# Kernel optimization log

Hardware: AMD Instinct MI355X
Metric: run time of the kernel (lower is better)

Reference implementation:

```python
import jax, jax.numpy as jnp
import numpy as np

K = 16  # nsample for knn_point

def _bn(x, g, b):
    # inference-mode BatchNorm1d folded to per-channel affine (running stats 0/1)
    return x * g[None, :, None] + b[None, :, None]

def _knn(xyz, k):
    # xyz: [B,3,N] -> idx [B,N,k] of k nearest neighbors (squared L2)
    p = xyz.transpose(0, 2, 1)                                   # [B,N,3]
    sq = jnp.sum(p * p, axis=-1)                                 # [B,N]
    d = sq[:, :, None] + sq[:, None, :] - 2.0 * jnp.einsum('bnc,bmc->bnm', p, p)
    _, idx = jax.lax.top_k(-d, k)
    return idx

def _gather(hT, idx):
    # hT: [B,N,C], idx: [B,N,K] -> [B,N,K,C]
    return jax.vmap(lambda a, i: a[i])(hT, idx)

def setup_inputs():
    key = jax.random.key(0)
    ks = jax.random.split(key, 12)
    B, N, C = 16, 2048, 128
    def w(k, shape, fan):
        return jax.random.normal(k, shape, jnp.float32) * (1.0 / np.sqrt(fan))
    o = jnp.ones; z = jnp.zeros
    return {
        'points': jax.random.normal(ks[0], (B, 6, N), jnp.float32),
        'label': jax.random.uniform(ks[1], (B, 1, 16), jnp.float32),
        'We1': w(ks[2], (C, 6), 6), 'ge1': o(C), 'be1': z(C),
        'We2': w(ks[3], (C, C), C), 'ge2': o(C), 'be2': z(C),
        'W1': w(ks[4], (3, C, C), C), 'g1': o((3, C)), 'b1': z((3, C)),
        'W2': w(ks[5], (3, C, C), C), 'g2': o((3, C)), 'b2': z((3, C)),
        'Wf': w(ks[6], (1024, 3 * C), 3 * C), 'gf': o(1024), 'bf': z(1024),
        'Wl': w(ks[7], (64, 16), 16), 'gl': o(64), 'bl': z(64),
        'Wc1': w(ks[8], (512, 3136), 3136), 'bc1': z(512), 'gc1': o(512), 'bb1': z(512),
        'Wc2': w(ks[9], (256, 512), 512), 'bc2': z(256), 'gc2': o(256), 'bb2': z(256),
        'Wc3': w(ks[10], (50, 256), 256), 'bc3': z(50),
    }

def reference(points, label, We1, ge1, be1, We2, ge2, be2, W1, g1, b1, W2, g2, b2,
              Wf, gf, bf, Wl, gl, bl, Wc1, bc1, gc1, bb1, Wc2, bc2, gc2, bb2, Wc3, bc3):
    B, _, N = points.shape
    x = points[:, :6, :]
    xyz = x[:, :3, :]
    idx = _knn(xyz, K)                                            # [B,N,16]
    # input embedding: two conv1x1 + BN + ReLU
    h = jax.nn.relu(_bn(jnp.einsum('oc,bcn->bon', We1, x), ge1, be1))
    h = jax.nn.relu(_bn(jnp.einsum('oc,bcn->bon', We2, h), ge2, be2))
    xs = []
    for i in range(3):  # PVDSA_Res blocks (simplified: conv-BN-ReLU, kNN max-agg, conv-BN + residual)
        t = jax.nn.relu(_bn(jnp.einsum('oc,bcn->bon', W1[i], h), g1[i], b1[i]))
        nbr = _gather(t.transpose(0, 2, 1), idx)                  # [B,N,K,C]
        m = nbr.max(axis=2).transpose(0, 2, 1)                    # [B,C,N]
        h = jax.nn.relu(_bn(jnp.einsum('oc,bcn->bon', W2[i], m), g2[i], b2[i]) + h)
        xs.append(h)
    xcat = jnp.concatenate(xs, axis=1)                            # [B,384,N]
    xf = jax.nn.leaky_relu(_bn(jnp.einsum('oc,bcn->bon', Wf, xcat), gf, bf), 0.2)  # [B,1024,N]
    x_max = xf.max(axis=-1)                                       # [B,1024]
    x_avg = xf.mean(axis=-1)                                      # [B,1024]
    cls = jnp.broadcast_to(label.transpose(0, 2, 1), (B, 16, N))
    lab = jax.nn.leaky_relu(_bn(jnp.einsum('oc,bcn->bon', Wl, cls), gl, bl), 0.2)  # [B,64,N]
    glob = jnp.concatenate([
        jnp.broadcast_to(x_max[:, :, None], (B, 1024, N)),
        jnp.broadcast_to(x_avg[:, :, None], (B, 1024, N)),
        lab], axis=1)
    xa = jnp.concatenate([xf, glob], axis=1)                      # [B,3136,N]
    c = jax.nn.relu(_bn(jnp.einsum('oc,bcn->bon', Wc1, xa) + bc1[None, :, None], gc1, bb1))
    c = jax.nn.relu(_bn(jnp.einsum('oc,bcn->bon', Wc2, c) + bc2[None, :, None], gc2, bb2))
    out = jnp.einsum('oc,bcn->bon', Wc3, c) + bc3[None, :, None]  # [B,50,N]
    return out
```

## Files before the change

kernel.cpp:

```cpp
#include <hip/hip_runtime.h>
#include <cstdint>
#include <cstddef>

#define DEVINL __device__ __forceinline__

typedef float    f32x4 __attribute__((ext_vector_type(4)));
typedef _Float16 f16x8 __attribute__((ext_vector_type(8)));
typedef _Float16 f16x4 __attribute__((ext_vector_type(4)));

constexpr int BB = 16, NN = 2048, MM = 32768;

constexpr size_t OFF_WE1 = 0;
constexpr size_t OFF_WE2 = OFF_WE1 + 128 * 64 * 2;
constexpr size_t OFF_W1  = OFF_WE2 + 128 * 128 * 2;
constexpr size_t OFF_W2  = OFF_W1  + 3 * 128 * 128 * 2;
constexpr size_t OFF_WF  = OFF_W2  + 3 * 128 * 128 * 2;
constexpr size_t OFF_WC1 = OFF_WF  + 1024 * 384 * 2;
constexpr size_t OFF_WC2 = OFF_WC1 + 512 * 1024 * 2;
constexpr size_t OFF_WC3 = OFF_WC2 + 256 * 512 * 2;
constexpr size_t OFF_BC2 = OFF_WC3 + 128 * 256 * 2;
constexpr size_t OFF_BC3 = OFF_BC2 + 256 * 4;
constexpr size_t OFF_CVEC= OFF_BC3 + 128 * 4;
constexpr size_t OFF_PMAX= OFF_CVEC+ 16 * 512 * 4;
constexpr size_t OFF_PSUM= OFF_PMAX+ 16 * 16 * 1024 * 4;
constexpr size_t OFF_IDX = OFF_PSUM+ 16 * 16 * 1024 * 4;
constexpr size_t OFF_R1  = 8ull << 20;
constexpr size_t OFF_X0  = OFF_R1;
constexpr size_t OFF_HT  = OFF_R1 + (4ull  << 20);
constexpr size_t OFF_TT  = OFF_R1 + (12ull << 20);
constexpr size_t OFF_MT  = OFF_R1 + (20ull << 20);
constexpr size_t OFF_C1  = OFF_R1;
constexpr size_t OFF_XCAT= OFF_R1 + (32ull << 20);
constexpr size_t OFF_C2  = OFF_XCAT;
constexpr size_t OFF_XF  = OFF_XCAT + (24ull << 20);

__global__ __launch_bounds__(256) void fold_all_kernel(
    const float* We1, const float* ge1, const float* We2, const float* ge2,
    const float* W1,  const float* g1,  const float* W2,  const float* g2,
    const float* Wf,  const float* gf,  const float* Wc1, const float* gc1,
    const float* Wc2, const float* gc2, const float* Wc3,
    const float* gc2b, const float* bc2, const float* bb2, const float* bc3,
    const float* pts, char* ws)
{
    const int bid = blockIdx.x;
    const int tid = threadIdx.x;

    if (bid == 4704) {
        ((float*)(ws + OFF_BC2))[tid] = gc2b[tid] * bc2[tid] + bb2[tid];
        return;
    }
    if (bid == 4705) {
        if (tid < 128) ((float*)(ws + OFF_BC3))[tid] = (tid < 50) ? bc3[tid] : 0.f;
        return;
    }
    if (bid >= 4706) {
        int m = (bid - 4706) * 256 + tid;
        int b = m >> 11, n = m & 2047;
        const float* ps = pts + (size_t)b * 6 * 2048 + n;
        _Float16 tmp[64];
#pragma unroll
        for (int c = 0; c < 64; ++c) tmp[c] = (_Float16)0.f;
#pragma unroll
        for (int c = 0; c < 6; ++c) tmp[c] = (_Float16)ps[(size_t)c << 11];
        _Float16* dst = (_Float16*)(ws + OFF_X0) + (size_t)m * 64;
#pragma unroll
        for (int v = 0; v < 8; ++v) *(f16x8*)(dst + v * 8) = *(const f16x8*)(tmp + v * 8);
        return;
    }

    int id, base;
    if      (bid < 32)   { id = 0;  base = 0;    }
    else if (bid < 96)   { id = 1;  base = 32;   }
    else if (bid < 160)  { id = 2;  base = 96;   }
    else if (bid < 224)  { id = 3;  base = 160;  }
    else if (bid < 288)  { id = 4;  base = 224;  }
    else if (bid < 352)  { id = 5;  base = 288;  }
    else if (bid < 416)  { id = 6;  base = 352;  }
    else if (bid < 480)  { id = 7;  base = 416;  }
    else if (bid < 2016) { id = 8;  base = 480;  }
    else if (bid < 4064) { id = 9;  base = 2016; }
    else if (bid < 4576) { id = 10; base = 4064; }
    else                 { id = 11; base = 4576; }

    const float* src = nullptr; const float* g = nullptr; _Float16* dst = nullptr;
    int O = 0, K = 0, lds = 0, Kp = 0;
    switch (id) {
        case 0:  src = We1; g = ge1; O = 128; K = 6;    lds = 6;    Kp = 64;   dst = (_Float16*)(ws + OFF_WE1); break;
        case 1:  src = We2; g = ge2; O = 128; K = 128;  lds = 128;  Kp = 128;  dst = (_Float16*)(ws + OFF_WE2); break;
        case 2: case 3: case 4: {
            int i = id - 2;
            src = W1 + (size_t)i * 16384; g = g1 + i * 128; O = 128; K = 128; lds = 128; Kp = 128;
            dst = (_Float16*)(ws + OFF_W1) + (size_t)i * 16384; break; }
        case 5: case 6: case 7: {
            int i = id - 5;
            src = W2 + (size_t)i * 16384; g = g2 + i * 128; O = 128; K = 128; lds = 128; Kp = 128;
            dst = (_Float16*)(ws + OFF_W2) + (size_t)i * 16384; break; }
        case 8:  src = Wf;  g = gf;  O = 1024; K = 384;  lds = 384;  Kp = 384;  dst = (_Float16*)(ws + OFF_WF);  break;
        case 9:  src = Wc1; g = gc1; O = 512;  K = 1024; lds = 3136; Kp = 1024; dst = (_Float16*)(ws + OFF_WC1); break;
        case 10: src = Wc2; g = gc2; O = 256;  K = 512;  lds = 512;  Kp = 512;  dst = (_Float16*)(ws + OFF_WC2); break;
        default: src = Wc3; g = nullptr; O = 50; K = 256; lds = 256; Kp = 256;  dst = (_Float16*)(ws + OFF_WC3); break;
    }
    int e = (bid - base) * 256 + tid;
    int o = e / Kp, k = e - o * Kp;
    float v = 0.f;
    if (o < O && k < K) {
        v = src[(size_t)o * lds + k];
        if (g) v *= g[o];
    }
    dst[e] = (_Float16)v;
}

DEVINL float knn_dist(const float4 pq, const float4 pm) {
    float t = pq.x * pm.x;
    t = fmaf(pq.y, pm.y, t);
    t = fmaf(pq.z, pm.z, t);
    return fmaf(-2.f, t, pm.w);
}

#define KNN_DINS(X) do { \
    const float x_ = (X); \
    d15 = __builtin_amdgcn_fmed3f(x_, d14, d15); \
    d14 = __builtin_amdgcn_fmed3f(x_, d13, d14); \
    d13 = __builtin_amdgcn_fmed3f(x_, d12, d13); \
    d12 = __builtin_amdgcn_fmed3f(x_, d11, d12); \
    d11 = __builtin_amdgcn_fmed3f(x_, d10, d11); \
    d10 = __builtin_amdgcn_fmed3f(x_, d9,  d10); \
    d9  = __builtin_amdgcn_fmed3f(x_, d8,  d9);  \
    d8  = __builtin_amdgcn_fmed3f(x_, d7,  d8);  \
    d7  = __builtin_amdgcn_fmed3f(x_, d6,  d7);  \
    d6  = __builtin_amdgcn_fmed3f(x_, d5,  d6);  \
    d5  = __builtin_amdgcn_fmed3f(x_, d4,  d5);  \
    d4  = __builtin_amdgcn_fmed3f(x_, d3,  d4);  \
    d3  = __builtin_amdgcn_fmed3f(x_, d2,  d3);  \
    d2  = __builtin_amdgcn_fmed3f(x_, d1,  d2);  \
    d1  = __builtin_amdgcn_fmed3f(x_, d0,  d1);  \
    d0  = __builtin_amdgcn_fmed3f(x_, -3.4e38f, d0); \
} while (0)

#define KNN_CE(A, B) { const float lo_ = fminf(A, B), hi_ = fmaxf(A, B); A = lo_; B = hi_; }

#define KNN_MERGE(OFF) do { \
    const float n0  = __shfl_xor(d0,  OFF), n1  = __shfl_xor(d1,  OFF), \
                n2  = __shfl_xor(d2,  OFF), n3  = __shfl_xor(d3,  OFF), \
                n4  = __shfl_xor(d4,  OFF), n5  = __shfl_xor(d5,  OFF), \
                n6  = __shfl_xor(d6,  OFF), n7  = __shfl_xor(d7,  OFF), \
                n8  = __shfl_xor(d8,  OFF), n9  = __shfl_xor(d9,  OFF), \
                n10 = __shfl_xor(d10, OFF), n11 = __shfl_xor(d11, OFF), \
                n12 = __shfl_xor(d12, OFF), n13 = __shfl_xor(d13, OFF), \
                n14 = __shfl_xor(d14, OFF), n15 = __shfl_xor(d15, OFF); \
    d0  = fminf(d0,  n15); d1  = fminf(d1,  n14); d2  = fminf(d2,  n13); d3  = fminf(d3,  n12); \
    d4  = fminf(d4,  n11); d5  = fminf(d5,  n10); d6  = fminf(d6,  n9);  d7  = fminf(d7,  n8);  \
    d8  = fminf(d8,  n7);  d9  = fminf(d9,  n6);  d10 = fminf(d10, n5);  d11 = fminf(d11, n4);  \
    d12 = fminf(d12, n3);  d13 = fminf(d13, n2);  d14 = fminf(d14, n1);  d15 = fminf(d15, n0);  \
    KNN_CE(d0, d8)  KNN_CE(d1, d9)  KNN_CE(d2, d10) KNN_CE(d3, d11) \
    KNN_CE(d4, d12) KNN_CE(d5, d13) KNN_CE(d6, d14) KNN_CE(d7, d15) \
    KNN_CE(d0, d4)  KNN_CE(d1, d5)  KNN_CE(d2, d6)  KNN_CE(d3, d7)  \
    KNN_CE(d8, d12) KNN_CE(d9, d13) KNN_CE(d10,d14) KNN_CE(d11,d15) \
    KNN_CE(d0, d2)  KNN_CE(d1, d3)  KNN_CE(d4, d6)  KNN_CE(d5, d7)  \
    KNN_CE(d8, d10) KNN_CE(d9, d11) KNN_CE(d12,d14) KNN_CE(d13,d15) \
    KNN_CE(d0, d1)  KNN_CE(d2, d3)  KNN_CE(d4, d5)  KNN_CE(d6, d7)  \
    KNN_CE(d8, d9)  KNN_CE(d10,d11) KNN_CE(d12,d13) KNN_CE(d14,d15) \
} while (0)

__global__ __launch_bounds__(256) void knn_kernel(const float* __restrict__ pts, int* __restrict__ idxout)
{
    __shared__ float4 P[2048];
    __shared__ unsigned short buf[32][96];
    __shared__ int cnt[32];
    __shared__ int wcnt[32];
    const int tid = threadIdx.x;
    const int b = blockIdx.x;
    const float* pb = pts + (size_t)b * 6 * 2048;
    for (int i = tid; i < 2048; i += 256) {
        float x = pb[i];
        float y = pb[2048 + i];
        float z = pb[4096 + i];
        P[i] = make_float4(x, y, z, x * x + y * y + z * z);
    }
    if (tid < 32) { cnt[tid] = 0; wcnt[tid] = 0; }
    __syncthreads();

    const int p = tid & 7;
    const int g = tid >> 3;
    const int q = blockIdx.y * 32 + g;
    const float4 pq = P[q];

    float d0 = 3.4e38f, d1 = 3.4e38f, d2 = 3.4e38f, d3 = 3.4e38f;
#pragma unroll 4
    for (int it = 0; it < 256; ++it) {
        const float4 pm = P[it * 8 + p];
        const float x = knn_dist(pq, pm);
        d3 = __builtin_amdgcn_fmed3f(x, d2, d3);
        d2 = __builtin_amdgcn_fmed3f(x, d1, d2);
        d1 = __builtin_amdgcn_fmed3f(x, d0, d1);
        d0 = fminf(x, d0);
    }
    float d4 = 3.4e38f, d5 = 3.4e38f, d6 = 3.4e38f, d7 = 3.4e38f,
          d8 = 3.4e38f, d9 = 3.4e38f, d10 = 3.4e38f, d11 = 3.4e38f,
          d12 = 3.4e38f, d13 = 3.4e38f, d14 = 3.4e38f, d15 = 3.4e38f;
    KNN_MERGE(1);
    KNN_MERGE(2);
    KNN_MERGE(4);
    const float tub = d15;

#pragma unroll 4
    for (int it = 0; it < 256; ++it) {
        const int m = it * 8 + p;
        const float d = knn_dist(pq, P[m]);
        if (d <= tub) {
            const int pos = atomicAdd(&cnt[g], 1);
            if (pos < 96) buf[g][pos] = (unsigned short)m;
        }
    }
    int C = cnt[g];
    if (C > 96) C = 96;

    d0 = 3.4e38f; d1 = 3.4e38f; d2 = 3.4e38f; d3 = 3.4e38f;
    d4 = 3.4e38f; d5 = 3.4e38f; d6 = 3.4e38f; d7 = 3.4e38f;
    d8 = 3.4e38f; d9 = 3.4e38f; d10 = 3.4e38f; d11 = 3.4e38f;
    d12 = 3.4e38f; d13 = 3.4e38f; d14 = 3.4e38f; d15 = 3.4e38f;
    for (int j = p; j < C; j += 8) {
        const int m = buf[g][j];
        const float x = knn_dist(pq, P[m]);
        KNN_DINS(x);
    }
    KNN_MERGE(1);
    KNN_MERGE(2);
    KNN_MERGE(4);
    const float t = d15;

    int* op = idxout + (((size_t)(b << 11) + q) << 4);
    for (int j = p; j < C; j += 8) {
        const int m = buf[g][j];
        const float d = knn_dist(pq, P[m]);
        if (d <= t) {
            const int pos = atomicAdd(&wcnt[g], 1);
            if (pos < 16) op[pos] = m;
        }
    }
}

template<int TM>
__global__ __launch_bounds__(256) void gemm_tile(
    const _Float16* __restrict__ W, const _Float16* __restrict__ X,
    _Float16* __restrict__ Y, float* __restrict__ Y32,
    const float* __restrict__ bias, const _Float16* __restrict__ Res,
    int Kp, int ldX, int xoff, int ldY, int yoff, int Opad,
    int act, int biasPerBatch, int ldR, int roff, int Olimit,
    float* __restrict__ pmax, float* __restrict__ psum)
{
    constexpr int MI = TM / 32;
    __shared__ _Float16 SH[128 * 64 + TM * 64];
    _Float16* As = SH;
    _Float16* Bs = SH + 128 * 64;

    const int tid  = threadIdx.x;
    const int lane = tid & 63, wave = tid >> 6;
    const int r = lane & 15, quad = lane >> 4;
    const int m_blk = blockIdx.x * TM, o_blk = blockIdx.y * 128;
    const int oh = (wave >> 1) * 64, mh = (wave & 1) * (TM / 2);

    f32x4 acc[4][MI];
#pragma unroll
    for (int a = 0; a < 4; ++a)
#pragma unroll
        for (int c = 0; c < MI; ++c) acc[a][c] = (f32x4){0.f, 0.f, 0.f, 0.f};

    const int srow  = wave * 8 + (lane >> 3);
    const int sslot = lane & 7;

    for (int k0 = 0; k0 < Kp; k0 += 64) {
        __syncthreads();
#pragma unroll
        for (int t = 0; t < 4; ++t) {
            const int rowA = t * 32 + srow;
            const int gk = k0 + ((sslot ^ (rowA & 7)) << 3);
            const _Float16* gA = W + (size_t)(o_blk + rowA) * Kp + gk;
            __builtin_amdgcn_global_load_lds(
                (const __attribute__((address_space(1))) unsigned int*)gA,
                (__attribute__((address_space(3))) unsigned int*)(As + t * 2048 + wave * 512),
                16, 0, 0);
        }
#pragma unroll
        for (int t = 0; t < TM / 32; ++t) {
            const int rowB = t * 32 + srow;
            const int gk = k0 + ((sslot ^ (rowB & 7)) << 3);
            const _Float16* gB = X + (size_t)(m_blk + rowB) * ldX + xoff + gk;
            __builtin_amdgcn_global_load_lds(
                (const __attribute__((address_space(1))) unsigned int*)gB,
                (__attribute__((address_space(3))) unsigned int*)(Bs + t * 2048 + wave * 512),
                16, 0, 0);
        }
        __syncthreads();
#pragma unroll
        for (int ks = 0; ks < 2; ++ks) {
            f16x8 af[4], bf[MI];
#pragma unroll
            for (int oi = 0; oi < 4; ++oi) {
                const int row = oh + oi * 16 + r;
                const int slot = (ks * 4 + quad) ^ (row & 7);
                af[oi] = *(const f16x8*)(As + row * 64 + slot * 8);
            }
#pragma unroll
            for (int mi = 0; mi < MI; ++mi) {
                const int row = mh + mi * 16 + r;
                const int slot = (ks * 4 + quad) ^ (row & 7);
                bf[mi] = *(const f16x8*)(Bs + row * 64 + slot * 8);
            }
#pragma unroll
            for (int oi = 0; oi < 4; ++oi)
#pragma unroll
                for (int mi = 0; mi < MI; ++mi)
                    acc[oi][mi] = __builtin_amdgcn_mfma_f32_16x16x32_f16(af[oi], bf[mi], acc[oi][mi], 0, 0, 0);
        }
    }

    const int bb = biasPerBatch ? (m_blk >> 11) * Opad : 0;
    __syncthreads();

    if (Y32) {
#pragma unroll
        for (int oi = 0; oi < 4; ++oi) {
            const int og = o_blk + oh + oi * 16 + quad * 4;
            const f32x4 bv = *(const f32x4*)(bias + bb + og);
#pragma unroll
            for (int mi = 0; mi < MI; ++mi) {
                const int m = m_blk + mh + mi * 16 + r;
                const int bidx = m >> 11, n = m & 2047;
                f32x4 v = acc[oi][mi] + bv;
#pragma unroll
                for (int j = 0; j < 4; ++j) {
                    float x = v[j];
                    if (act == 1)      x = (x > 0.f) ? x : 0.0f;
                    else if (act == 2) x = (x > 0.f) ? x : 0.2f * x;
                    const int o = og + j;
                    if (o < Olimit)
                        Y32[((size_t)(bidx * 50 + o) << 11) + n] = x;
                }
            }
        }
        return;
    }

    _Float16* OT = SH;
#pragma unroll
    for (int oi = 0; oi < 4; ++oi) {
        const int ol = oh + oi * 16 + quad * 4;
        const f32x4 bv = *(const f32x4*)(bias + bb + o_blk + ol);
#pragma unroll
        for (int mi = 0; mi < MI; ++mi) {
            const int row = mh + mi * 16 + r;
            f32x4 v = acc[oi][mi] + bv;
            if (Res) {
                f16x4 rr = *(const f16x4*)(Res + (size_t)(m_blk + row) * ldR + roff + o_blk + ol);
#pragma unroll
                for (int j = 0; j < 4; ++j) v[j] += (float)rr[j];
            }
            f16x4 ov;
#pragma unroll
            for (int j = 0; j < 4; ++j) {
                float x = v[j];
                if (act == 1)      x = (x > 0.f) ? x : 0.0f;
                else if (act == 2) x = (x > 0.f) ? x : 0.2f * x;
                ov[j] = (_Float16)x;
            }
            const int s = ((ol >> 2) ^ (row & 31)) << 2;
            *(f16x4*)(OT + row * 128 + s) = ov;
        }
    }
    __syncthreads();
#pragma unroll
    for (int it2 = 0; it2 < TM / 16; ++it2) {
        const int row = it2 * 16 + (tid >> 4);
        const int c = tid & 15;
        const int s0 = ((c * 2) ^ (row & 31)) << 2;
        const int s1 = ((c * 2 + 1) ^ (row & 31)) << 2;
        f16x4 a = *(const f16x4*)(OT + row * 128 + s0);
        f16x4 b2 = *(const f16x4*)(OT + row * 128 + s1);
        f16x8 o8;
        o8[0] = a[0]; o8[1] = a[1]; o8[2] = a[2]; o8[3] = a[3];
        o8[4] = b2[0]; o8[5] = b2[1]; o8[6] = b2[2]; o8[7] = b2[3];
        *(f16x8*)(Y + (size_t)(m_blk + row) * ldY + yoff + o_blk + c * 8) = o8;
    }

    if constexpr (TM == 128) {
        if (pmax) {
            const int cg = tid & 31, h = tid >> 5;
            float mx0 = -3.4e38f, mx1 = -3.4e38f, mx2 = -3.4e38f, mx3 = -3.4e38f;
            float sm0 = 0.f, sm1 = 0.f, sm2 = 0.f, sm3 = 0.f;
#pragma unroll
            for (int rr = 0; rr < 16; ++rr) {
                const int r2 = h * 16 + rr;
                const f16x4 v = *(const f16x4*)(OT + r2 * 128 + ((cg ^ (r2 & 31)) << 2));
                const float x0 = (float)v[0], x1 = (float)v[1], x2 = (float)v[2], x3 = (float)v[3];
                mx0 = fmaxf(mx0, x0); sm0 += x0;
                mx1 = fmaxf(mx1, x1); sm1 += x1;
                mx2 = fmaxf(mx2, x2); sm2 += x2;
                mx3 = fmaxf(mx3, x3); sm3 += x3;
            }
            __syncthreads();
            float* PR = (float*)SH;
            float* pw = PR + (size_t)(h * 128 + cg * 4) * 2;
            pw[0] = mx0; pw[1] = sm0; pw[2] = mx1; pw[3] = sm1;
            pw[4] = mx2; pw[5] = sm2; pw[6] = mx3; pw[7] = sm3;
            __syncthreads();
            if (tid < 128) {
                float M = -3.4e38f, S = 0.f;
#pragma unroll
                for (int h2 = 0; h2 < 8; ++h2) {
                    M = fmaxf(M, PR[(size_t)(h2 * 128 + tid) * 2]);
                    S += PR[(size_t)(h2 * 128 + tid) * 2 + 1];
                }
                const int b2 = m_blk >> 11, mt = (m_blk >> 7) & 15;
                pmax[((size_t)(b2 * 16 + mt) << 10) + o_blk + tid] = M;
                psum[((size_t)(b2 * 16 + mt) << 10) + o_blk + tid] = S;
            }
        }
    }
}

typedef short s16x8 __attribute__((ext_vector_type(8)));
__global__ __launch_bounds__(256) void gather_max_kernel(
    const short* __restrict__ T, const int* __restrict__ idx, short* __restrict__ Mo)
{
    const int tid = threadIdx.x;
    const int p = blockIdx.x * 16 + (tid >> 4);
    const int l = tid & 15;
    const int b = p >> 11;
    const int* ip = idx + (size_t)p * 16;
    size_t row = (size_t)((b << 11) + ip[0]);
    s16x8 cur = *(const s16x8*)(T + row * 128 + l * 8);
    unsigned short best[8];
#pragma unroll
    for (int e = 0; e < 8; ++e) best[e] = (unsigned short)cur[e];
#pragma unroll
    for (int j = 1; j < 16; ++j) {
        row = (size_t)((b << 11) + ip[j]);
        s16x8 v = *(const s16x8*)(T + row * 128 + l * 8);
#pragma unroll
        for (int e = 0; e < 8; ++e) {
            unsigned short u = (unsigned short)v[e];
            if (u > best[e]) best[e] = u;
        }
    }
    s16x8 ov;
#pragma unroll
    for (int e = 0; e < 8; ++e) ov[e] = (short)best[e];
    *(s16x8*)(Mo + (size_t)p * 128 + l * 8) = ov;
}

__global__ __launch_bounds__(256) void cvec_kernel(
    const float* __restrict__ label, const float* __restrict__ Wl, const float* __restrict__ gl, const float* __restrict__ bl,
    const float* __restrict__ Wc1, const float* __restrict__ bc1, const float* __restrict__ gc1, const float* __restrict__ bb1,
    const float* __restrict__ pmax, const float* __restrict__ psum, float* __restrict__ cvec)
{
    __shared__ float v[2112];
    __shared__ float red[256];
    const int b = blockIdx.x, og = blockIdx.y, tid = threadIdx.x;
    for (int i = tid; i < 1024; i += 256) {
        float mx = -3.4e38f, sm = 0.f;
#pragma unroll
        for (int c = 0; c < 16; ++c) {
            mx = fmaxf(mx, pmax[((size_t)(b * 16 + c) << 10) + i]);
            sm += psum[((size_t)(b * 16 + c) << 10) + i];
        }
        v[i] = mx;
        v[1024 + i] = sm * (1.f / 2048.f);
    }
    if (tid < 64) {
        float s = 0.f;
        for (int i = 0; i < 16; ++i) s += Wl[tid * 16 + i] * label[b * 16 + i];
        s = gl[tid] * s + bl[tid];
        v[2048 + tid] = (s > 0.f) ? s : 0.2f * s;
    }
    __syncthreads();
    const int o = og * 64 + (tid >> 2), part = tid & 3;
    const float* wrow = Wc1 + (size_t)o * 3136 + 1024 + part * 528;
    float s = 0.f;
    for (int j = 0; j < 528; ++j) s += wrow[j] * v[part * 528 + j];
    red[tid] = s;
    __syncthreads();
    if (part == 0) {
        float tot = red[tid] + red[tid + 1] + red[tid + 2] + red[tid + 3];
        cvec[((size_t)b << 9) + o] = gc1[o] * (tot + bc1[o]) + bb1[o];
    }
}

extern "C" void kernel_launch(void* const* d_in, const int* in_sizes, int n_in,
                              void* d_out, int out_size, void* d_ws, size_t ws_size,
                              hipStream_t stream)
{
    (void)in_sizes; (void)n_in; (void)out_size; (void)ws_size;
    const float* points = (const float*)d_in[0];
    const float* label  = (const float*)d_in[1];
    const float* We1 = (const float*)d_in[2];
    const float* ge1 = (const float*)d_in[3];
    const float* be1 = (const float*)d_in[4];
    const float* We2 = (const float*)d_in[5];
    const float* ge2 = (const float*)d_in[6];
    const float* be2 = (const float*)d_in[7];
    const float* W1  = (const float*)d_in[8];
    const float* g1  = (const float*)d_in[9];
    const float* b1  = (const float*)d_in[10];
    const float* W2  = (const float*)d_in[11];
    const float* g2  = (const float*)d_in[12];
    const float* b2  = (const float*)d_in[13];
    const float* Wf  = (const float*)d_in[14];
    const float* gf  = (const float*)d_in[15];
    const float* bfv = (const float*)d_in[16];
    const float* Wl  = (const float*)d_in[17];
    const float* gl  = (const float*)d_in[18];
    const float* bl  = (const float*)d_in[19];
    const float* Wc1 = (const float*)d_in[20];
    const float* bc1 = (const float*)d_in[21];
    const float* gc1 = (const float*)d_in[22];
    const float* bb1 = (const float*)d_in[23];
    const float* Wc2 = (const float*)d_in[24];
    const float* bc2 = (const float*)d_in[25];
    const float* gc2 = (const float*)d_in[26];
    const float* bb2 = (const float*)d_in[27];
    const float* Wc3 = (const float*)d_in[28];
    const float* bc3 = (const float*)d_in[29];

    char* ws = (char*)d_ws;
    _Float16* hT  = (_Float16*)(ws + OFF_HT);
    _Float16* tT  = (_Float16*)(ws + OFF_TT);
    _Float16* mT  = (_Float16*)(ws + OFF_MT);
    _Float16* xct = (_Float16*)(ws + OFF_XCAT);
    _Float16* xf  = (_Float16*)(ws + OFF_XF);
    _Float16* c1  = (_Float16*)(ws + OFF_C1);
    _Float16* c2  = (_Float16*)(ws + OFF_C2);
    int*      idx = (int*)     (ws + OFF_IDX);
    _Float16* x0  = (_Float16*)(ws + OFF_X0);

    _Float16* wE1 = (_Float16*)(ws + OFF_WE1);
    _Float16* wE2 = (_Float16*)(ws + OFF_WE2);
    _Float16* w1f = (_Float16*)(ws + OFF_W1);
    _Float16* w2f = (_Float16*)(ws + OFF_W2);
    _Float16* wF  = (_Float16*)(ws + OFF_WF);
    _Float16* wC1 = (_Float16*)(ws + OFF_WC1);
    _Float16* wC2 = (_Float16*)(ws + OFF_WC2);
    _Float16* wC3 = (_Float16*)(ws + OFF_WC3);
    float* bC2 = (float*)(ws + OFF_BC2);
    float* bC3 = (float*)(ws + OFF_BC3);
    float* cv  = (float*)(ws + OFF_CVEC);
    float* pmx = (float*)(ws + OFF_PMAX);
    float* psm = (float*)(ws + OFF_PSUM);

    fold_all_kernel<<<dim3(4834), 256, 0, stream>>>(We1, ge1, We2, ge2, W1, g1, W2, g2,
                                                    Wf, gf, Wc1, gc1, Wc2, gc2, Wc3,
                                                    gc2, bc2, bb2, bc3, points, ws);
    knn_kernel<<<dim3(BB, NN / 32), 256, 0, stream>>>(points, idx);

    gemm_tile<64><<<dim3(512, 1), 256, 0, stream>>>(wE1, x0, tT, nullptr, be1, nullptr, 64, 64, 0, 128, 0, 128, 1, 0, 0, 0, 128, nullptr, nullptr);
    gemm_tile<64><<<dim3(512, 1), 256, 0, stream>>>(wE2, tT, hT, nullptr, be2, nullptr, 128, 128, 0, 128, 0, 128, 1, 0, 0, 0, 128, nullptr, nullptr);

    for (int i = 0; i < 3; ++i) {
        const _Float16* hin = (i == 0) ? hT : xct;
        int ldH  = (i == 0) ? 128 : 384;
        int offH = (i == 0) ? 0 : (i - 1) * 128;
        gemm_tile<64><<<dim3(512, 1), 256, 0, stream>>>(w1f + (size_t)i * 16384, hin, tT, nullptr, b1 + i * 128, nullptr,
                                                        128, ldH, offH, 128, 0, 128, 1, 0, 0, 0, 128, nullptr, nullptr);
        gather_max_kernel<<<dim3(MM / 16), 256, 0, stream>>>((const short*)tT, idx, (short*)mT);
        gemm_tile<64><<<dim3(512, 1), 256, 0, stream>>>(w2f + (size_t)i * 16384, mT, xct, nullptr, b2 + i * 128, hin,
                                                        128, 128, 0, 384, i * 128, 128, 1, 0, ldH, offH, 128, nullptr, nullptr);
    }

    gemm_tile<128><<<dim3(256, 8), 256, 0, stream>>>(wF, xct, xf, nullptr, bfv, nullptr, 384, 384, 0, 1024, 0, 1024, 2, 0, 0, 0, 1024, pmx, psm);

    cvec_kernel<<<dim3(BB, 8), 256, 0, stream>>>(label, Wl, gl, bl, Wc1, bc1, gc1, bb1, pmx, psm, cv);

    gemm_tile<128><<<dim3(256, 4), 256, 0, stream>>>(wC1, xf, c1, nullptr, cv, nullptr, 1024, 1024, 0, 512, 0, 512, 1, 1, 0, 0, 512, nullptr, nullptr);
    gemm_tile<128><<<dim3(256, 2), 256, 0, stream>>>(wC2, c1, c2, nullptr, bC2, nullptr, 512, 512, 0, 256, 0, 256, 1, 0, 0, 0, 256, nullptr, nullptr);
    gemm_tile<128><<<dim3(256, 1), 256, 0, stream>>>(wC3, c2, nullptr, (float*)d_out, bC3, nullptr, 256, 256, 0, 0, 0, 128, 0, 0, 0, 0, 50, nullptr, nullptr);
}
```

Measured before the change: 419.2 us.

## Double-buffer LDS tiles in GEMM to overlap global loads with MFMA

The GEMM kernel now keeps two LDS stages for the A/B tiles and issues the async global-to-LDS loads for the next K tile before computing the current one. Partial vmcnt waits let the current stage's loads complete while the next stage's loads stay in flight, hiding load latency behind MFMA work. It also raises wave priority during the MFMA section. LDS usage doubles, which may reduce occupancy, and the hand-counted vmcnt values must match the number of loads issued per stage.

```diff
diff --git a/kernel.cpp b/kernel.cpp
--- a/kernel.cpp
+++ b/kernel.cpp
@@ -250,9 +250,9 @@
     float* __restrict__ pmax, float* __restrict__ psum)
 {
     constexpr int MI = TM / 32;
-    __shared__ _Float16 SH[128 * 64 + TM * 64];
-    _Float16* As = SH;
-    _Float16* Bs = SH + 128 * 64;
+    constexpr int ASZ = 128 * 64;
+    constexpr int BSZ = TM * 64;
+    __shared__ _Float16 SH[2 * (ASZ + BSZ)];
 
     const int tid  = threadIdx.x;
     const int lane = tid & 63, wave = tid >> 6;
@@ -269,8 +269,9 @@
     const int srow  = wave * 8 + (lane >> 3);
     const int sslot = lane & 7;
 
-    for (int k0 = 0; k0 < Kp; k0 += 64) {
-        __syncthreads();
+    auto STAGE = [&](int bufi, int k0) {
+        _Float16* As = SH + bufi * (ASZ + BSZ);
+        _Float16* Bs = As + ASZ;
 #pragma unroll
         for (int t = 0; t < 4; ++t) {
             const int rowA = t * 32 + srow;
@@ -291,7 +292,26 @@
                 (__attribute__((address_space(3))) unsigned int*)(Bs + t * 2048 + wave * 512),
                 16, 0, 0);
         }
-        __syncthreads();
+    };
+
+    const int nt = Kp >> 6;
+    STAGE(0, 0);
+    int cur = 0;
+    for (int t = 0; t < nt; ++t) {
+        if (t + 1 < nt) {
+            STAGE(cur ^ 1, (t + 1) << 6);
+            if constexpr (TM == 128) asm volatile("s_waitcnt vmcnt(8)" ::: "memory");
+            else                     asm volatile("s_waitcnt vmcnt(6)" ::: "memory");
+        } else {
+            asm volatile("s_waitcnt vmcnt(0)" ::: "memory");
+        }
+        __builtin_amdgcn_sched_barrier(0);
+        __builtin_amdgcn_s_barrier();
+        asm volatile("" ::: "memory");
+
+        const _Float16* As = SH + cur * (ASZ + BSZ);
+        const _Float16* Bs = As + ASZ;
+        __builtin_amdgcn_s_setprio(1);
 #pragma unroll
         for (int ks = 0; ks < 2; ++ks) {
             f16x8 af[4], bf[MI];
@@ -313,6 +333,10 @@
                 for (int mi = 0; mi < MI; ++mi)
                     acc[oi][mi] = __builtin_amdgcn_mfma_f32_16x16x32_f16(af[oi], bf[mi], acc[oi][mi], 0, 0, 0);
         }
+        __builtin_amdgcn_s_setprio(0);
+        asm volatile("" ::: "memory");
+        __builtin_amdgcn_s_barrier();
+        cur ^= 1;
     }
 
     const int bb = biasPerBatch ? (m_blk >> 11) * Opad : 0;
```

Result: no change. 414.6 us (-1.1%).
